# Kernel tuning notes

Hardware: AMD Instinct MI355X
Metric: run time of the kernel (lower is better)

## Reference

```python
import jax, jax.numpy as jnp
import numpy as np

N_NODES = 100000   # n_nodes in data_config
K = 32             # edge_threshold (neighbors per node)
D = 64             # in_channel == out_channel == emb_size, heads = 1
B = 1024           # index batch size
NEG_SLOPE = 0.2


def setup_inputs() -> dict:
    key = jax.random.key(0)
    ks = jax.random.split(key, 10)
    glorot = (6.0 / (D + D)) ** 0.5
    all_embed = jax.random.normal(ks[0], (N_NODES, D), jnp.float32) * 0.1     # xavier-ish
    W = jax.random.uniform(ks[1], (D, D), jnp.float32, -glorot, glorot)       # GATConv.weight (heads*out = 64)
    g_att = (6.0 / (1 + 2 * D)) ** 0.5
    att = jax.random.uniform(ks[2], (1, 1, 2 * D), jnp.float32, -g_att, g_att)  # GATConv.att
    bias = jnp.zeros((D,), jnp.float32)                                       # GATConv.bias (zeros init)
    edges_matrix = jax.random.randint(ks[3], (N_NODES, K), 0, N_NODES)
    user = jax.random.randint(ks[4], (B,), 0, 10000)
    pos_item = jax.random.randint(ks[5], (B,), 0, N_NODES)
    neg_item = jax.random.randint(ks[6], (B,), 0, N_NODES)
    pos_rules = jax.random.randint(ks[7], (B,), 0, N_NODES)
    selected_neg_outfits_rules = jax.random.randint(ks[8], (B,), 0, N_NODES)
    return {
        "all_embed": all_embed, "W": W, "att": att, "bias": bias,
        "user": user, "pos_item": pos_item, "neg_item": neg_item,
        "edges_matrix": edges_matrix, "pos_rules": pos_rules,
        "selected_neg_outfits_rules": selected_neg_outfits_rules,
    }


def reference(all_embed, W, att, bias, user, pos_item, neg_item,
              edges_matrix, pos_rules, selected_neg_outfits_rules):
    n, d = all_embed.shape
    k = edges_matrix.shape[1]

    # build_edge: src = repeated node index, dst = neighbor index; then edges.t()
    # -> edge_index[0] = source j, edge_index[1] = target i (PyG source_to_target)
    src = jnp.repeat(jnp.arange(n), k)          # [N*K]
    dst = edges_matrix.reshape(-1)              # [N*K]
    valid = src != dst                          # remove_self_loops (mask, static shape)
    loop = jnp.arange(n)                        # add_self_loops
    src = jnp.concatenate([src, loop])          # [E], E = N*K + N
    dst = jnp.concatenate([dst, loop])
    valid = jnp.concatenate([valid, jnp.ones((n,), bool)])

    # x = mm(x, W).view(-1, heads=1, out=64)
    h = all_embed @ W                           # [N, D]

    # alpha = sum(cat([x_i, x_j], -1) * att, -1); precontract att with h (cheap)
    a_i = att[0, 0, :d]                         # target half
    a_j = att[0, 0, d:]                         # source half
    s_i = h @ a_i                               # [N]
    s_j = h @ a_j                               # [N]
    alpha = s_i[dst] + s_j[src]                 # [E]
    alpha = jnp.where(alpha >= 0, alpha, NEG_SLOPE * alpha)  # leaky_relu
    alpha = jnp.where(valid, alpha, -1e9)       # removed self-loop edges drop out of softmax

    # segment softmax over target nodes (every node has a self loop -> no empty segment)
    m = jax.lax.stop_gradient(jax.ops.segment_max(alpha, dst, num_segments=n))
    e = jnp.exp(alpha - m[dst])
    denom = jax.ops.segment_sum(e, dst, num_segments=n)
    a = e / (denom[dst] + 1e-16)                # [E]

    # message = x_j * alpha ; aggregate = scatter-add at targets
    out = jax.ops.segment_sum(h[src] * a[:, None], dst, num_segments=n)  # [N, D]

    # update: mean over heads (1 head -> identity) + bias
    out = out + bias

    # GraphConv_KGAT: dropout (identity in eval) then F.normalize (L2, eps=1e-12)
    norm = jnp.linalg.norm(out, axis=-1, keepdims=True)
    gcn_embedding = out / jnp.maximum(norm, 1e-12)
    return gcn_embedding
```

## Files before the change

### kernel.cpp

```cpp
#include <hip/hip_runtime.h>
#include <hip/hip_bf16.h>

#define NEG_SLOPE 0.2f
#define BSHIFT 8
#define BSIZE  (1 << BSHIFT)
#define CAP    9216
#define NBMAX  400
#define SRC_MASK 0x1FFFF

typedef float v2f __attribute__((ext_vector_type(2)));

__device__ __forceinline__ float lrelu(float x) { return fmaxf(x, NEG_SLOPE * x); }
__device__ __forceinline__ float bf2f(unsigned short u) {
    return __uint_as_float((unsigned)u << 16);
}
__device__ __forceinline__ unsigned short f2bf(float f) {
    unsigned u = __float_as_uint(f);
    return (unsigned short)((u + 0x7fffu + ((u >> 16) & 1u)) >> 16);
}

__global__ __launch_bounds__(256, 4) void k_gemm(
    const float* __restrict__ A, const float* __restrict__ W,
    const float* __restrict__ att,
    unsigned short* __restrict__ h16, float* __restrict__ s_i, float* __restrict__ s_j, int n)
{
    __shared__ float At[64 * 68];
    __shared__ float Wl[64 * 68];
    const int tid  = threadIdx.x;
    const int lane = tid & 63;
    const int tx = tid & 15, ty = tid >> 4;
    const int r0 = ty * 4, c0 = tx * 4;
    const long row0 = (long)blockIdx.x * 64;

    {
        int r = tid & 63;
        int kb = (tid >> 6) * 4;
        long gr = row0 + r; if (gr >= n) gr = n - 1;
        const float4* Ar = (const float4*)(A + gr * 64);
#pragma unroll
        for (int p = 0; p < 4; ++p) {
            int k0 = p * 16 + kb;
            float4 a = Ar[k0 >> 2];
            At[(k0 + 0) * 68 + r] = a.x;
            At[(k0 + 1) * 68 + r] = a.y;
            At[(k0 + 2) * 68 + r] = a.z;
            At[(k0 + 3) * 68 + r] = a.w;
        }
        int c = (tid & 15) * 4;
        int rr = tid >> 4;
#pragma unroll
        for (int p = 0; p < 4; ++p) {
            int k = rr + p * 16;
            *(float4*)&Wl[k * 68 + c] = *(const float4*)(W + k * 64 + c);
        }
    }
    __syncthreads();

    float acc[4][4] = {};
#pragma unroll 4
    for (int k = 0; k < 64; ++k) {
        float4 a = *(const float4*)&At[k * 68 + r0];
        float4 w = *(const float4*)&Wl[k * 68 + c0];
        acc[0][0] = fmaf(a.x, w.x, acc[0][0]);
        acc[0][1] = fmaf(a.x, w.y, acc[0][1]);
        acc[0][2] = fmaf(a.x, w.z, acc[0][2]);
        acc[0][3] = fmaf(a.x, w.w, acc[0][3]);
        acc[1][0] = fmaf(a.y, w.x, acc[1][0]);
        acc[1][1] = fmaf(a.y, w.y, acc[1][1]);
        acc[1][2] = fmaf(a.y, w.z, acc[1][2]);
        acc[1][3] = fmaf(a.y, w.w, acc[1][3]);
        acc[2][0] = fmaf(a.z, w.x, acc[2][0]);
        acc[2][1] = fmaf(a.z, w.y, acc[2][1]);
        acc[2][2] = fmaf(a.z, w.z, acc[2][2]);
        acc[2][3] = fmaf(a.z, w.w, acc[2][3]);
        acc[3][0] = fmaf(a.w, w.x, acc[3][0]);
        acc[3][1] = fmaf(a.w, w.y, acc[3][1]);
        acc[3][2] = fmaf(a.w, w.z, acc[3][2]);
        acc[3][3] = fmaf(a.w, w.w, acc[3][3]);
    }

    const int rowlim = (int)(((long)n - row0) < 64 ? (n - row0) : 64);

#pragma unroll
    for (int i = 0; i < 4; ++i) {
        int r = r0 + i;
        if (r < rowlim) {
            uint2 uv;
            uv.x = (unsigned)f2bf(acc[i][0]) | ((unsigned)f2bf(acc[i][1]) << 16);
            uv.y = (unsigned)f2bf(acc[i][2]) | ((unsigned)f2bf(acc[i][3]) << 16);
            *(uint2*)(h16 + (row0 + r) * 64 + c0) = uv;
        }
    }

    float4 avi = *(const float4*)(att + c0);
    float4 avj = *(const float4*)(att + 64 + c0);
#pragma unroll
    for (int i = 0; i < 4; ++i) {
        float pi = acc[i][0] * avi.x;
        pi = fmaf(acc[i][1], avi.y, pi);
        pi = fmaf(acc[i][2], avi.z, pi);
        pi = fmaf(acc[i][3], avi.w, pi);
        float pj = acc[i][0] * avj.x;
        pj = fmaf(acc[i][1], avj.y, pj);
        pj = fmaf(acc[i][2], avj.z, pj);
        pj = fmaf(acc[i][3], avj.w, pj);
#pragma unroll
        for (int o = 1; o <= 8; o <<= 1) {
            pi += __shfl_xor(pi, o, 64);
            pj += __shfl_xor(pj, o, 64);
        }
        int r = r0 + i;
        if ((lane & 15) == 0 && r < rowlim) {
            s_i[row0 + r] = pi;
            s_j[row0 + r] = pj;
        }
    }
}

__global__ __launch_bounds__(512) void k_binA(
    const int* __restrict__ edges, int* __restrict__ bcursor,
    unsigned* __restrict__ pairs, int n_edges, int nb)
{
    __shared__ int hist[512];
    __shared__ int st[512];
    __shared__ int cur[512];
    __shared__ int gbase[512];
    __shared__ int wsum[8];
    __shared__ unsigned lp[8192];
    const int t = threadIdx.x;
    const int w = t >> 6, lane = t & 63;
    const long base = (long)blockIdx.x * 8192;

    int er[16];
#pragma unroll
    for (int k = 0; k < 16; ++k) {
        long e = base + k * 512 + t;
        int d = -1;
        if (e < n_edges) {
            d = edges[e];
            if (d == (int)(e >> 5)) d = -1;
        }
        er[k] = d;
    }

    hist[t] = 0;
    __syncthreads();
#pragma unroll
    for (int k = 0; k < 16; ++k)
        if (er[k] >= 0) atomicAdd(&hist[er[k] >> BSHIFT], 1);
    __syncthreads();

    int hv = hist[t];
    int inc = hv;
#pragma unroll
    for (int off = 1; off < 64; off <<= 1) {
        int u = __shfl_up(inc, off, 64);
        if (lane >= off) inc += u;
    }
    if (lane == 63) wsum[w] = inc;
    __syncthreads();
    {
        int wb_ = 0;
        for (int i = 0; i < w; ++i) wb_ += wsum[i];
        int s0 = inc - hv + wb_;
        st[t] = s0;
        cur[t] = s0;
        gbase[t] = 0;
    }
    if (t < nb && hist[t] > 0) gbase[t] = atomicAdd(&bcursor[t], hist[t]);
    __syncthreads();

#pragma unroll
    for (int k = 0; k < 16; ++k) {
        int d = er[k];
        if (d >= 0) {
            int b = d >> BSHIFT;
            int slot = atomicAdd(&cur[b], 1);
            long e = base + k * 512 + t;
            lp[slot] = ((unsigned)(d & (BSIZE - 1)) << 17) | (unsigned)(e >> 5);
        }
    }
    __syncthreads();

    for (int b = w; b < nb; b += 8) {
        int cnt = hist[b];
        int gb  = gbase[b];
        int cw  = cnt;
        if (gb + cw > CAP) cw = CAP - gb;
        long gdst = (long)b * CAP + gb;
        int sb = st[b];
        for (int s = lane; s < cw; s += 64)
            pairs[gdst + s] = lp[sb + s];
    }
}

__global__ __launch_bounds__(512) void k_binB(
    const int* __restrict__ bcursor, unsigned* __restrict__ pairs,
    int* __restrict__ offs, int* __restrict__ counts, int n)
{
    __shared__ unsigned pl[CAP];
    __shared__ unsigned srt[CAP];
    __shared__ int hist[BSIZE];
    __shared__ int cur[BSIZE];
    __shared__ int wsum[4];
    int b = blockIdx.x, t = threadIdx.x;
    const int w = t >> 6, lane = t & 63;
    int cnt = bcursor[b];
    if (cnt > CAP) cnt = CAP;
    long wb = (long)b * CAP;

    for (int s = t; s < cnt; s += 512) pl[s] = pairs[wb + s];
    if (t < BSIZE) hist[t] = 0;
    __syncthreads();
    for (int s = t; s < cnt; s += 512) atomicAdd(&hist[pl[s] >> 17], 1);
    __syncthreads();

    int hv = (t < BSIZE) ? hist[t] : 0;
    int inc = hv;
#pragma unroll
    for (int off = 1; off < 64; off <<= 1) {
        int u = __shfl_up(inc, off, 64);
        if (lane >= off) inc += u;
    }
    if (t < BSIZE && lane == 63) wsum[w] = inc;
    __syncthreads();
    if (t < BSIZE) {
        int wb_ = 0;
        for (int i = 0; i < w; ++i) wb_ += wsum[i];
        int start = inc - hv + wb_;
        int dg = (b << BSHIFT) + t;
        if (dg < n) {
            offs[dg]   = (int)(wb + start);
            counts[dg] = hv;
        }
        cur[t] = start;
    }
    __syncthreads();

    for (int s = t; s < cnt; s += 512) {
        unsigned pk = pl[s];
        int pos = atomicAdd(&cur[pk >> 17], 1);
        srt[pos] = pk & SRC_MASK;
    }
    __syncthreads();

    for (int s = t; s < cnt; s += 512)
        ((int*)pairs)[wb + s] = (int)srt[s];
}

__global__ __launch_bounds__(256) void k_gather(
    const int* __restrict__ offs, const int* __restrict__ counts,
    const int* __restrict__ srcl, const unsigned short* __restrict__ h16,
    const float* __restrict__ s_i, const float* __restrict__ s_j,
    const float* __restrict__ bias, float* __restrict__ out, int n)
{
    int gw = (blockIdx.x * 256 + threadIdx.x) >> 6;
    int lane = threadIdx.x & 63;
    if (gw >= n) return;
    const int d = gw;
    const int off = offs[d], deg = counts[d];
    const float si = s_i[d];
    const float es = __expf(lrelu(si + s_j[d]));

    const int g  = lane >> 3;
    const int li = lane & 7;
    const char* hb = (const char*)h16 + (li << 4);

    v2f acc2[4];
#pragma unroll
    for (int i = 0; i < 4; ++i) acc2[i] = (v2f)0.f;
    float denp = 0.f;

    for (int base = 0; base < deg; base += 64) {
        int t = base + lane;
        int cnt = min(64, deg - base);
        int soff = 0; float w = 0.f;
        if (t < deg) {
            int s = srcl[off + t];
            soff = s << 7;
            w = __expf(lrelu(si + s_j[s]));
        }
        denp += w;
        for (int j = 0; j < cnt; j += 16) {
            int i0 = j + g, i1 = j + 8 + g;
            float w0 = __shfl(w, i0, 64);
            int   o0 = __shfl(soff, i0, 64);
            float w1 = __shfl(w, i1, 64);
            int   o1 = __shfl(soff, i1, 64);
            uint4 ha = *(const uint4*)(hb + o0);
            uint4 hc = *(const uint4*)(hb + o1);
            v2f w0v = {w0, w0};
            v2f w1v = {w1, w1};
            v2f p;
            p = (v2f){__uint_as_float(ha.x << 16), __uint_as_float(ha.x & 0xffff0000u)};
            acc2[0] += p * w0v;
            p = (v2f){__uint_as_float(ha.y << 16), __uint_as_float(ha.y & 0xffff0000u)};
            acc2[1] += p * w0v;
            p = (v2f){__uint_as_float(ha.z << 16), __uint_as_float(ha.z & 0xffff0000u)};
            acc2[2] += p * w0v;
            p = (v2f){__uint_as_float(ha.w << 16), __uint_as_float(ha.w & 0xffff0000u)};
            acc2[3] += p * w0v;
            p = (v2f){__uint_as_float(hc.x << 16), __uint_as_float(hc.x & 0xffff0000u)};
            acc2[0] += p * w1v;
            p = (v2f){__uint_as_float(hc.y << 16), __uint_as_float(hc.y & 0xffff0000u)};
            acc2[1] += p * w1v;
            p = (v2f){__uint_as_float(hc.z << 16), __uint_as_float(hc.z & 0xffff0000u)};
            acc2[2] += p * w1v;
            p = (v2f){__uint_as_float(hc.w << 16), __uint_as_float(hc.w & 0xffff0000u)};
            acc2[3] += p * w1v;
        }
    }

    float acc[8];
    acc[0] = acc2[0].x; acc[1] = acc2[0].y;
    acc[2] = acc2[1].x; acc[3] = acc2[1].y;
    acc[4] = acc2[2].x; acc[5] = acc2[2].y;
    acc[6] = acc2[3].x; acc[7] = acc2[3].y;

#pragma unroll
    for (int o = 8; o <= 32; o <<= 1) {
#pragma unroll
        for (int i = 0; i < 8; ++i)
            acc[i] += __shfl_xor(acc[i], o, 64);
    }
#pragma unroll
    for (int o = 32; o; o >>= 1) denp += __shfl_xor(denp, o, 64);

    uint4 hd = *(const uint4*)(hb + (d << 7));
    float den = denp + es + 1e-16f;
    float rden = 1.f / den;
    const float4* pb = (const float4*)(bias + (li << 3));
    float4 b0 = pb[0], b1 = pb[1];

    float v[8];
    v[0] = fmaf(__uint_as_float(hd.x << 16),         es, acc[0]) * rden + b0.x;
    v[1] = fmaf(__uint_as_float(hd.x & 0xffff0000u), es, acc[1]) * rden + b0.y;
    v[2] = fmaf(__uint_as_float(hd.y << 16),         es, acc[2]) * rden + b0.z;
    v[3] = fmaf(__uint_as_float(hd.y & 0xffff0000u), es, acc[3]) * rden + b0.w;
    v[4] = fmaf(__uint_as_float(hd.z << 16),         es, acc[4]) * rden + b1.x;
    v[5] = fmaf(__uint_as_float(hd.z & 0xffff0000u), es, acc[5]) * rden + b1.y;
    v[6] = fmaf(__uint_as_float(hd.w << 16),         es, acc[6]) * rden + b1.z;
    v[7] = fmaf(__uint_as_float(hd.w & 0xffff0000u), es, acc[7]) * rden + b1.w;

    float sq = 0.f;
#pragma unroll
    for (int i = 0; i < 8; ++i) sq = fmaf(v[i], v[i], sq);
#pragma unroll
    for (int o = 1; o <= 4; o <<= 1) sq += __shfl_xor(sq, o, 64);
    float rn = 1.f / fmaxf(sqrtf(sq), 1e-12f);

    if (g < 2) {
        float4 ov;
        if (g == 0) ov = make_float4(v[0] * rn, v[1] * rn, v[2] * rn, v[3] * rn);
        else        ov = make_float4(v[4] * rn, v[5] * rn, v[6] * rn, v[7] * rn);
        *(float4*)(out + ((long)d << 6) + (li << 3) + (g << 2)) = ov;
    }
}

extern "C" void kernel_launch(void* const* d_in, const int* in_sizes, int n_in,
                              void* d_out, int out_size, void* d_ws, size_t ws_size,
                              hipStream_t stream)
{
    const float* A    = (const float*)d_in[0];
    const float* W    = (const float*)d_in[1];
    const float* att  = (const float*)d_in[2];
    const float* bias = (const float*)d_in[3];
    const int* edges  = (const int*)d_in[7];

    int n = in_sizes[0] / 64;
    int n_edges = in_sizes[7];
    int nb = (n + BSIZE - 1) >> BSHIFT;

    unsigned short* h16 = (unsigned short*)d_ws;
    float* s_i      = (float*)(h16 + (long)n * 64);
    float* s_j      = s_i + n;
    int* offs       = (int*)(s_j + n);
    int* counts     = offs + n;
    int* bcursor    = counts + n;
    unsigned* pairs = (unsigned*)(bcursor + 512);

    (void)hipMemsetAsync(bcursor, 0, 512 * sizeof(int), stream);

    int blocks_rows = (n + 63) / 64;
    k_gemm<<<blocks_rows, 256, 0, stream>>>(A, W, att, h16, s_i, s_j, n);

    int blocks_binA = (n_edges + 8191) / 8192;
    k_binA<<<blocks_binA, 512, 0, stream>>>(edges, bcursor, pairs, n_edges, nb);

    k_binB<<<nb, 512, 0, stream>>>(bcursor, pairs, offs, counts, n);

    int blocks_waves = ((long)n * 64 + 255) / 256;
    k_gather<<<blocks_waves, 256, 0, stream>>>(offs, counts, (const int*)pairs, h16,
                                               s_i, s_j, bias, (float*)d_out, n);
}
```

Baseline: 215.6 us.

## Fuse GEMM and edge binning into one launch with block-role dispatch

Merges the projection GEMM kernel and the first edge-binning kernel into a single kernel. The first blocks do binning and the remaining blocks do the GEMM, with shared memory unioned between the two roles. This removes one launch and lets the two independent stages run concurrently on the GPU. The GEMM blocks move to 512 threads with 2 rows per thread, which raises register-tile overhead per output. Binning adds an extra barrier because wsum now aliases gbase.

```diff
diff --git a/kernel.cpp b/kernel.cpp
--- a/kernel.cpp
+++ b/kernel.cpp
@@ -19,178 +19,170 @@
     return (unsigned short)((u + 0x7fffu + ((u >> 16) & 1u)) >> 16);
 }
 
-__global__ __launch_bounds__(256, 4) void k_gemm(
+__global__ __launch_bounds__(512, 8) void k_front(
     const float* __restrict__ A, const float* __restrict__ W,
     const float* __restrict__ att,
-    unsigned short* __restrict__ h16, float* __restrict__ s_i, float* __restrict__ s_j, int n)
+    unsigned short* __restrict__ h16, float* __restrict__ s_i, float* __restrict__ s_j, int n,
+    const int* __restrict__ edges, int* __restrict__ bcursor,
+    unsigned* __restrict__ pairs, int n_edges, int nb, int nba)
 {
-    __shared__ float At[64 * 68];
-    __shared__ float Wl[64 * 68];
-    const int tid  = threadIdx.x;
-    const int lane = tid & 63;
-    const int tx = tid & 15, ty = tid >> 4;
-    const int r0 = ty * 4, c0 = tx * 4;
-    const long row0 = (long)blockIdx.x * 64;
-
-    {
-        int r = tid & 63;
-        int kb = (tid >> 6) * 4;
-        long gr = row0 + r; if (gr >= n) gr = n - 1;
-        const float4* Ar = (const float4*)(A + gr * 64);
-#pragma unroll
-        for (int p = 0; p < 4; ++p) {
-            int k0 = p * 16 + kb;
-            float4 a = Ar[k0 >> 2];
-            At[(k0 + 0) * 68 + r] = a.x;
-            At[(k0 + 1) * 68 + r] = a.y;
-            At[(k0 + 2) * 68 + r] = a.z;
-            At[(k0 + 3) * 68 + r] = a.w;
-        }
-        int c = (tid & 15) * 4;
-        int rr = tid >> 4;
-#pragma unroll
-        for (int p = 0; p < 4; ++p) {
-            int k = rr + p * 16;
-            *(float4*)&Wl[k * 68 + c] = *(const float4*)(W + k * 64 + c);
-        }
-    }
-    __syncthreads();
-
-    float acc[4][4] = {};
+    __shared__ union {
+        struct { float At[64 * 68]; float Wl[64 * 68]; } g;
+        struct { int hist[512]; int st[512]; int cur[512];
+                 int gbase[512]; unsigned lp[8192]; } b;
+    } sh;
+    const int t = threadIdx.x;
+
+    if ((int)blockIdx.x < nba) {
+        int* hist = sh.b.hist; int* st = sh.b.st; int* cur = sh.b.cur;
+        int* gbase = sh.b.gbase; unsigned* lp = sh.b.lp;
+        int* wsum = gbase + 504;
+        const int w = t >> 6, lane = t & 63;
+        const long base = (long)blockIdx.x * 8192;
+
+        int er[16];
+#pragma unroll
+        for (int k = 0; k < 16; ++k) {
+            long e = base + k * 512 + t;
+            int d = -1;
+            if (e < n_edges) {
+                d = edges[e];
+                if (d == (int)(e >> 5)) d = -1;
+            }
+            er[k] = d;
+        }
+
+        hist[t] = 0;
+        __syncthreads();
+#pragma unroll
+        for (int k = 0; k < 16; ++k)
+            if (er[k] >= 0) atomicAdd(&hist[er[k] >> BSHIFT], 1);
+        __syncthreads();
+
+        int hv = hist[t];
+        int inc = hv;
+#pragma unroll
+        for (int off = 1; off < 64; off <<= 1) {
+            int u = __shfl_up(inc, off, 64);
+            if (lane >= off) inc += u;
+        }
+        if (lane == 63) wsum[w] = inc;
+        __syncthreads();
+        {
+            int wb_ = 0;
+            for (int i = 0; i < w; ++i) wb_ += wsum[i];
+            int s0 = inc - hv + wb_;
+            st[t] = s0;
+            cur[t] = s0;
+            if (t < NBMAX) gbase[t] = 0;
+        }
+        __syncthreads();
+        if (t < nb && hist[t] > 0) gbase[t] = atomicAdd(&bcursor[t], hist[t]);
+        __syncthreads();
+
+#pragma unroll
+        for (int k = 0; k < 16; ++k) {
+            int d = er[k];
+            if (d >= 0) {
+                int b = d >> BSHIFT;
+                int slot = atomicAdd(&cur[b], 1);
+                long e = base + k * 512 + t;
+                lp[slot] = ((unsigned)(d & (BSIZE - 1)) << 17) | (unsigned)(e >> 5);
+            }
+        }
+        __syncthreads();
+
+        for (int b = w; b < nb; b += 8) {
+            int cnt = hist[b];
+            int gb  = gbase[b];
+            int cw  = cnt;
+            if (gb + cw > CAP) cw = CAP - gb;
+            long gdst = (long)b * CAP + gb;
+            int sb = st[b];
+            for (int s = lane; s < cw; s += 64)
+                pairs[gdst + s] = lp[sb + s];
+        }
+    } else {
+        float* At = sh.g.At; float* Wl = sh.g.Wl;
+        const int lane = t & 63;
+        const int tx = t & 15, ty = t >> 4;
+        const int r0 = ty * 2, c0 = tx * 4;
+        const long row0 = (long)(blockIdx.x - nba) * 64;
+
+        {
+            int r = t & 63;
+            int kb = (t >> 6) * 4;
+            long gr = row0 + r; if (gr >= n) gr = n - 1;
+            const float4* Ar = (const float4*)(A + gr * 64);
+#pragma unroll
+            for (int p = 0; p < 2; ++p) {
+                int k0 = p * 32 + kb;
+                float4 a = Ar[k0 >> 2];
+                At[(k0 + 0) * 68 + r] = a.x;
+                At[(k0 + 1) * 68 + r] = a.y;
+                At[(k0 + 2) * 68 + r] = a.z;
+                At[(k0 + 3) * 68 + r] = a.w;
+            }
+            int rr = t >> 4;
+#pragma unroll
+            for (int p = 0; p < 2; ++p) {
+                int k = rr + p * 32;
+                *(float4*)&Wl[k * 68 + c0] = *(const float4*)(W + k * 64 + c0);
+            }
+        }
+        __syncthreads();
+
+        float acc[2][4] = {};
 #pragma unroll 4
-    for (int k = 0; k < 64; ++k) {
-        float4 a = *(const float4*)&At[k * 68 + r0];
-        float4 w = *(const float4*)&Wl[k * 68 + c0];
-        acc[0][0] = fmaf(a.x, w.x, acc[0][0]);
-        acc[0][1] = fmaf(a.x, w.y, acc[0][1]);
-        acc[0][2] = fmaf(a.x, w.z, acc[0][2]);
-        acc[0][3] = fmaf(a.x, w.w, acc[0][3]);
-        acc[1][0] = fmaf(a.y, w.x, acc[1][0]);
-        acc[1][1] = fmaf(a.y, w.y, acc[1][1]);
-        acc[1][2] = fmaf(a.y, w.z, acc[1][2]);
-        acc[1][3] = fmaf(a.y, w.w, acc[1][3]);
-        acc[2][0] = fmaf(a.z, w.x, acc[2][0]);
-        acc[2][1] = fmaf(a.z, w.y, acc[2][1]);
-        acc[2][2] = fmaf(a.z, w.z, acc[2][2]);
-        acc[2][3] = fmaf(a.z, w.w, acc[2][3]);
-        acc[3][0] = fmaf(a.w, w.x, acc[3][0]);
-        acc[3][1] = fmaf(a.w, w.y, acc[3][1]);
-        acc[3][2] = fmaf(a.w, w.z, acc[3][2]);
-        acc[3][3] = fmaf(a.w, w.w, acc[3][3]);
-    }
-
-    const int rowlim = (int)(((long)n - row0) < 64 ? (n - row0) : 64);
-
-#pragma unroll
-    for (int i = 0; i < 4; ++i) {
-        int r = r0 + i;
-        if (r < rowlim) {
-            uint2 uv;
-            uv.x = (unsigned)f2bf(acc[i][0]) | ((unsigned)f2bf(acc[i][1]) << 16);
-            uv.y = (unsigned)f2bf(acc[i][2]) | ((unsigned)f2bf(acc[i][3]) << 16);
-            *(uint2*)(h16 + (row0 + r) * 64 + c0) = uv;
-        }
-    }
-
-    float4 avi = *(const float4*)(att + c0);
-    float4 avj = *(const float4*)(att + 64 + c0);
-#pragma unroll
-    for (int i = 0; i < 4; ++i) {
-        float pi = acc[i][0] * avi.x;
-        pi = fmaf(acc[i][1], avi.y, pi);
-        pi = fmaf(acc[i][2], avi.z, pi);
-        pi = fmaf(acc[i][3], avi.w, pi);
-        float pj = acc[i][0] * avj.x;
-        pj = fmaf(acc[i][1], avj.y, pj);
-        pj = fmaf(acc[i][2], avj.z, pj);
-        pj = fmaf(acc[i][3], avj.w, pj);
-#pragma unroll
-        for (int o = 1; o <= 8; o <<= 1) {
-            pi += __shfl_xor(pi, o, 64);
-            pj += __shfl_xor(pj, o, 64);
-        }
-        int r = r0 + i;
-        if ((lane & 15) == 0 && r < rowlim) {
-            s_i[row0 + r] = pi;
-            s_j[row0 + r] = pj;
-        }
-    }
-}
-
-__global__ __launch_bounds__(512) void k_binA(
-    const int* __restrict__ edges, int* __restrict__ bcursor,
-    unsigned* __restrict__ pairs, int n_edges, int nb)
-{
-    __shared__ int hist[512];
-    __shared__ int st[512];
-    __shared__ int cur[512];
-    __shared__ int gbase[512];
-    __shared__ int wsum[8];
-    __shared__ unsigned lp[8192];
-    const int t = threadIdx.x;
-    const int w = t >> 6, lane = t & 63;
-    const long base = (long)blockIdx.x * 8192;
-
-    int er[16];
-#pragma unroll
-    for (int k = 0; k < 16; ++k) {
-        long e = base + k * 512 + t;
-        int d = -1;
-        if (e < n_edges) {
-            d = edges[e];
-            if (d == (int)(e >> 5)) d = -1;
-        }
-        er[k] = d;
-    }
-
-    hist[t] = 0;
-    __syncthreads();
-#pragma unroll
-    for (int k = 0; k < 16; ++k)
-        if (er[k] >= 0) atomicAdd(&hist[er[k] >> BSHIFT], 1);
-    __syncthreads();
-
-    int hv = hist[t];
-    int inc = hv;
-#pragma unroll
-    for (int off = 1; off < 64; off <<= 1) {
-        int u = __shfl_up(inc, off, 64);
-        if (lane >= off) inc += u;
-    }
-    if (lane == 63) wsum[w] = inc;
-    __syncthreads();
-    {
-        int wb_ = 0;
-        for (int i = 0; i < w; ++i) wb_ += wsum[i];
-        int s0 = inc - hv + wb_;
-        st[t] = s0;
-        cur[t] = s0;
-        gbase[t] = 0;
-    }
-    if (t < nb && hist[t] > 0) gbase[t] = atomicAdd(&bcursor[t], hist[t]);
-    __syncthreads();
-
-#pragma unroll
-    for (int k = 0; k < 16; ++k) {
-        int d = er[k];
-        if (d >= 0) {
-            int b = d >> BSHIFT;
-            int slot = atomicAdd(&cur[b], 1);
-            long e = base + k * 512 + t;
-            lp[slot] = ((unsigned)(d & (BSIZE - 1)) << 17) | (unsigned)(e >> 5);
-        }
-    }
-    __syncthreads();
-
-    for (int b = w; b < nb; b += 8) {
-        int cnt = hist[b];
-        int gb  = gbase[b];
-        int cw  = cnt;
-        if (gb + cw > CAP) cw = CAP - gb;
-        long gdst = (long)b * CAP + gb;
-        int sb = st[b];
-        for (int s = lane; s < cw; s += 64)
-            pairs[gdst + s] = lp[sb + s];
+        for (int k = 0; k < 64; ++k) {
+            float2 a = *(const float2*)&At[k * 68 + r0];
+            float4 w4 = *(const float4*)&Wl[k * 68 + c0];
+            acc[0][0] = fmaf(a.x, w4.x, acc[0][0]);
+            acc[0][1] = fmaf(a.x, w4.y, acc[0][1]);
+            acc[0][2] = fmaf(a.x, w4.z, acc[0][2]);
+            acc[0][3] = fmaf(a.x, w4.w, acc[0][3]);
+            acc[1][0] = fmaf(a.y, w4.x, acc[1][0]);
+            acc[1][1] = fmaf(a.y, w4.y, acc[1][1]);
+            acc[1][2] = fmaf(a.y, w4.z, acc[1][2]);
+            acc[1][3] = fmaf(a.y, w4.w, acc[1][3]);
+        }
+
+        const int rowlim = (int)(((long)n - row0) < 64 ? (n - row0) : 64);
+
+#pragma unroll
+        for (int i = 0; i < 2; ++i) {
+            int r = r0 + i;
+            if (r < rowlim) {
+                uint2 uv;
+                uv.x = (unsigned)f2bf(acc[i][0]) | ((unsigned)f2bf(acc[i][1]) << 16);
+                uv.y = (unsigned)f2bf(acc[i][2]) | ((unsigned)f2bf(acc[i][3]) << 16);
+                *(uint2*)(h16 + (row0 + r) * 64 + c0) = uv;
+            }
+        }
+
+        float4 avi = *(const float4*)(att + c0);
+        float4 avj = *(const float4*)(att + 64 + c0);
+#pragma unroll
+        for (int i = 0; i < 2; ++i) {
+            float pi = acc[i][0] * avi.x;
+            pi = fmaf(acc[i][1], avi.y, pi);
+            pi = fmaf(acc[i][2], avi.z, pi);
+            pi = fmaf(acc[i][3], avi.w, pi);
+            float pj = acc[i][0] * avj.x;
+            pj = fmaf(acc[i][1], avj.y, pj);
+            pj = fmaf(acc[i][2], avj.z, pj);
+            pj = fmaf(acc[i][3], avj.w, pj);
+#pragma unroll
+            for (int o = 1; o <= 8; o <<= 1) {
+                pi += __shfl_xor(pi, o, 64);
+                pj += __shfl_xor(pj, o, 64);
+            }
+            int r = r0 + i;
+            if ((lane & 15) == 0 && r < rowlim) {
+                s_i[row0 + r] = pi;
+                s_j[row0 + r] = pj;
+            }
+        }
     }
 }
 
@@ -382,10 +374,9 @@
     (void)hipMemsetAsync(bcursor, 0, 512 * sizeof(int), stream);
 
     int blocks_rows = (n + 63) / 64;
-    k_gemm<<<blocks_rows, 256, 0, stream>>>(A, W, att, h16, s_i, s_j, n);
-
     int blocks_binA = (n_edges + 8191) / 8192;
-    k_binA<<<blocks_binA, 512, 0, stream>>>(edges, bcursor, pairs, n_edges, nb);
+    k_front<<<blocks_binA + blocks_rows, 512, 0, stream>>>(
+        A, W, att, h16, s_i, s_j, n, edges, bcursor, pairs, n_edges, nb, blocks_binA);
 
     k_binB<<<nb, 512, 0, stream>>>(bcursor, pairs, offs, counts, n);
 
```

Measured after the change: 197.8 us. -8.3%, faster.
